# Kernel optimization log

Hardware: AMD Instinct MI355X
Metric: run time of the kernel (lower is better)

Reference implementation:

```python
import jax, jax.numpy as jnp
import numpy as np

EPS = 1e-5

def _leaky(x):
    return jax.nn.leaky_relu(x, 0.2)

def _bn(x, p, axis):
    # p: [4, C] rows = (gamma, beta, running_mean, running_var); inference-mode BN
    g, b, m, v = p
    scale = g * jax.lax.rsqrt(v + EPS)
    shape = [1] * x.ndim
    shape[axis] = -1
    return x * scale.reshape(shape) + (b - m * scale).reshape(shape)

def _graph_feature(x, k):
    # x: [B, C, N] -> edge features [B, 2C, N, k] (knn on -squared-distance, topk largest)
    B, C, N = x.shape
    xx = jnp.sum(x * x, axis=1)                                   # [B, N]
    pd = 2.0 * jnp.einsum('bcn,bcm->bnm', x, x) - xx[:, :, None] - xx[:, None, :]
    idx = jax.lax.top_k(pd, k)[1]                                 # [B, N, k]
    xt = jnp.transpose(x, (0, 2, 1))                              # [B, N, C]
    nb = xt[jnp.arange(B)[:, None, None], idx]                    # [B, N, k, C]
    ctr = xt[:, :, None, :]
    f = jnp.concatenate([nb - ctr, jnp.broadcast_to(ctr, nb.shape)], axis=-1)
    return jnp.transpose(f, (0, 3, 1, 2))                         # [B, 2C, N, k]

def _cbam(x, fc1, fc2, sw):
    # Channel attention (shared MLP on avg+max pooled) then spatial attention (5x5 conv)
    mlp = lambda v: jax.nn.relu(v @ fc1.T) @ fc2.T
    ca = jax.nn.sigmoid(mlp(jnp.mean(x, (2, 3))) + mlp(jnp.max(x, (2, 3))))
    x = x * ca[:, :, None, None]
    s = jnp.concatenate([jnp.mean(x, 1, keepdims=True), jnp.max(x, 1, keepdims=True)], axis=1)
    sa = jax.lax.conv_general_dilated(s, sw, (1, 1), [(2, 2), (2, 2)],
                                      dimension_numbers=('NCHW', 'OIHW', 'NCHW'))
    return x * jax.nn.sigmoid(sa)

def _edge_block(x, k, W, bn, fc1, fc2, sw):
    f = _graph_feature(x, k)                                      # [B, 2C, N, k]
    f = _leaky(_bn(jnp.einsum('oc,bcnk->bonk', W, f), bn, 1))     # 1x1 conv + BN + LeakyReLU
    f = _cbam(f, fc1, fc2, sw)
    return jnp.max(f, axis=-1)                                    # [B, Cout, N]

def _bn_params(key, c):
    k1, k2, k3, k4 = jax.random.split(key, 4)
    g = 1.0 + 0.1 * jax.random.normal(k1, (c,))
    b = 0.1 * jax.random.normal(k2, (c,))
    m = 0.1 * jax.random.normal(k3, (c,))
    v = 0.5 + jax.random.uniform(k4, (c,))
    return jnp.stack([g, b, m, v])

def setup_inputs() -> dict:
    key = jax.random.key(0)
    nrm = lambda i, shape, s: s * jax.random.normal(jax.random.fold_in(key, i), shape, dtype=jnp.float32)
    d = {}
    d['x'] = jax.random.normal(jax.random.fold_in(key, 0), (4, 3, 2048), dtype=jnp.float32)
    d['W1'] = nrm(1, (64, 6), 0.3)
    d['W2'] = nrm(2, (64, 128), 0.15)
    d['W3'] = nrm(3, (128, 128), 0.15)
    d['W4'] = nrm(4, (256, 256), 0.1)
    d['W5'] = nrm(5, (1024, 512), 0.08)
    for i, c in zip(range(1, 6), [64, 64, 128, 256, 1024]):
        d['bn%d' % i] = _bn_params(jax.random.fold_in(key, 10 + i), c)
    d['bn6'] = _bn_params(jax.random.fold_in(key, 16), 512)
    d['bn7'] = _bn_params(jax.random.fold_in(key, 17), 256)
    for j, c in zip(range(1, 5), [64, 64, 128, 256]):
        r = c // 8
        d['ca%d_fc1' % j] = nrm(20 + j, (r, c), 0.2)
        d['ca%d_fc2' % j] = nrm(30 + j, (c, r), 0.2)
        d['sa%d' % j] = nrm(40 + j, (1, 2, 5, 5), 0.2)
    d['lin1_w'] = nrm(50, (512, 2048), 0.05)
    d['lin2_w'] = nrm(51, (256, 512), 0.08)
    d['lin2_b'] = nrm(52, (256,), 0.05)
    d['lin3_w'] = nrm(53, (40, 256), 0.1)
    d['lin3_b'] = nrm(54, (40,), 0.05)
    d['k'] = 20
    return d

def reference(x, W1, bn1, ca1_fc1, ca1_fc2, sa1, W2, bn2, ca2_fc1, ca2_fc2, sa2,
              W3, bn3, ca3_fc1, ca3_fc2, sa3, W4, bn4, ca4_fc1, ca4_fc2, sa4,
              W5, bn5, lin1_w, bn6, lin2_w, lin2_b, bn7, lin3_w, lin3_b, k):
    x1 = _edge_block(x,  k, W1, bn1, ca1_fc1, ca1_fc2, sa1)   # [B, 64, N]
    x2 = _edge_block(x1, k, W2, bn2, ca2_fc1, ca2_fc2, sa2)   # [B, 64, N]
    x3 = _edge_block(x2, k, W3, bn3, ca3_fc1, ca3_fc2, sa3)   # [B, 128, N]
    x4 = _edge_block(x3, k, W4, bn4, ca4_fc1, ca4_fc2, sa4)   # [B, 256, N]
    xc = jnp.concatenate([x1, x2, x3, x4], axis=1)            # [B, 512, N]
    h = _leaky(_bn(jnp.einsum('oc,bcn->bon', W5, xc), bn5, 1))  # [B, 1024, N]
    g = jnp.concatenate([jnp.max(h, axis=-1), jnp.mean(h, axis=-1)], axis=1)  # [B, 2048]
    g = _leaky(_bn(g @ lin1_w.T, bn6, 1))                     # dropout = identity (eval)
    g = _leaky(_bn(g @ lin2_w.T + lin2_b, bn7, 1))
    return g @ lin3_w.T + lin3_b                              # [B, 40]
```

## Files before the change

### kernel.cpp

```cpp
#include <hip/hip_runtime.h>
#include <math.h>

#define BB 4
#define NN 2048
#define KK 20
#define EPSF 1e-5f
#define TR 4

__device__ __forceinline__ float leaky(float x){ return x > 0.f ? x : 0.2f*x; }
__device__ __forceinline__ float sigm(float x){ return 1.f/(1.f+expf(-x)); }

__global__ void k_xx(const float* __restrict__ X, long bstride, int C, float* __restrict__ xx){
  int i = blockIdx.x*blockDim.x + threadIdx.x;
  int b = i >> 11, n = i & (NN-1);
  const float* xb = X + (long)b*bstride;
  float s = 0.f;
  for (int c = 0; c < C; ++c){ float v = xb[c*NN + n]; s += v*v; }
  xx[i] = s;
}

__global__ __launch_bounds__(256) void k_knn(const float* __restrict__ X, long bstride, int C,
                      const float* __restrict__ xx, int* __restrict__ idx){
  __shared__ unsigned int pdrow[TR][NN];
  int rowsPerB = NN/TR;
  int b = blockIdx.x / rowsPerB;
  int r0 = (blockIdx.x % rowsPerB) * TR;
  const float* xb = X + (long)b*bstride;
  int tid = threadIdx.x;

  float acc[4][8];
  #pragma unroll
  for (int r = 0; r < 4; ++r)
    #pragma unroll
    for (int j = 0; j < 8; ++j) acc[r][j] = 0.f;
  for (int c = 0; c < C; ++c){
    const float* xcp = xb + (long)c*NN;
    float4 ctr = *(const float4*)(xcp + r0);
    float v[8];
    #pragma unroll
    for (int j = 0; j < 8; ++j) v[j] = xcp[tid + 256*j];
    #pragma unroll
    for (int j = 0; j < 8; ++j){
      acc[0][j] = fmaf(ctr.x, v[j], acc[0][j]);
      acc[1][j] = fmaf(ctr.y, v[j], acc[1][j]);
      acc[2][j] = fmaf(ctr.z, v[j], acc[2][j]);
      acc[3][j] = fmaf(ctr.w, v[j], acc[3][j]);
    }
  }
  float xxr[4];
  #pragma unroll
  for (int r = 0; r < 4; ++r) xxr[r] = xx[b*NN + r0 + r];
  #pragma unroll
  for (int j = 0; j < 8; ++j){
    int m = tid + 256*j;
    float xxm = xx[b*NN + m];
    #pragma unroll
    for (int r = 0; r < 4; ++r){
      float pd = 2.f*acc[r][j] - xxr[r] - xxm;
      unsigned u = __float_as_uint(pd);
      u ^= (u & 0x80000000u) ? 0xFFFFFFFFu : 0x80000000u;
      pdrow[r][m] = u;
    }
  }
  __syncthreads();

  int wave = tid >> 6, lane = tid & 63;
  int r = wave;
  unsigned long long k1 = 0ull, k2 = 0ull;
  #pragma unroll
  for (int j = 0; j < 32; ++j){
    int m = lane + (j<<6);
    unsigned long long key = ((unsigned long long)pdrow[r][m] << 11) | (unsigned)(2047 - m);
    if (key > k1){ k2 = k1; k1 = key; }
    else if (key > k2){ k2 = key; }
  }
  unsigned removed = 0u;
  int* orow = idx + ((long)b*NN + r0 + r)*KK;
  for (int sel = 0; sel < KK; ++sel){
    unsigned long long g = k1;
    #pragma unroll
    for (int off = 32; off; off >>= 1){
      unsigned long long o = __shfl_xor(g, off);
      if (o > g) g = o;
    }
    int gm = 2047 - (int)(g & 2047u);
    if (lane == 0) orow[sel] = gm;
    if ((gm & 63) == lane){
      removed |= 1u << (gm >> 6);
      k1 = k2; k2 = 0ull;
      if (k1 == 0ull){
        #pragma unroll
        for (int j = 0; j < 32; ++j){
          if (removed & (1u << j)) continue;
          int m = lane + (j<<6);
          unsigned long long key = ((unsigned long long)pdrow[r][m] << 11) | (unsigned)(2047 - m);
          if (key > k1){ k2 = k1; k1 = key; }
          else if (key > k2){ k2 = key; }
        }
      }
    }
  }
}

__global__ void k_proj(const float* __restrict__ X, long bstride, int C, int Cout,
                       const float* __restrict__ W, const float* __restrict__ bn,
                       float* __restrict__ Pg, float* __restrict__ PgT,
                       float* __restrict__ Pc, float* __restrict__ PcT){
  int nb = NN/256;
  int t = blockIdx.x;
  int nchunk = t % nb; t /= nb;
  int o = t % Cout; int b = t / Cout;
  int m = nchunk*256 + threadIdx.x;
  const float* xb = X + (long)b*bstride;
  float a1 = 0.f, a2 = 0.f;
  for (int c = 0; c < C; ++c){
    float v  = xb[c*NN + m];
    float wl = W[o*2*C + c], wr = W[o*2*C + C + c];
    a1 += wl*v; a2 += (wr - wl)*v;
  }
  float gg = bn[o], bb = bn[Cout+o], mn = bn[2*Cout+o], vv = bn[3*Cout+o];
  float scale = gg * rsqrtf(vv + EPSF);
  float bias  = bb - mn*scale;
  float pg = scale*a1;
  float pc = scale*a2 + bias;
  Pg [((long)b*Cout + o)*NN + m] = pg;
  PgT[((long)b*NN + m)*Cout + o] = pg;
  Pc [((long)b*Cout + o)*NN + m] = pc;
  PcT[((long)b*NN + m)*Cout + o] = pc;
}

__global__ void k_cstats(const float* __restrict__ Pg, const float* __restrict__ Pc,
                         const int* __restrict__ idx, int Cout,
                         float* __restrict__ cmean, float* __restrict__ cmax){
  int b = blockIdx.x / Cout, o = blockIdx.x % Cout;
  const float* pg = Pg + ((long)b*Cout + o)*NN;
  const float* pc = Pc + ((long)b*Cout + o)*NN;
  const int* id = idx + (long)b*NN*KK;
  int tid = threadIdx.x;
  float s = 0.f, mx = -INFINITY;
  for (int i = tid; i < NN*KK; i += 256){
    int n = i / KK;
    int iv = id[i];
    float v = leaky(pg[iv] + pc[n]);
    s += v; mx = fmaxf(mx, v);
  }
  __shared__ float ss[256], sm[256];
  ss[tid] = s; sm[tid] = mx; __syncthreads();
  for (int st = 128; st; st >>= 1){
    if (tid < st){ ss[tid] += ss[tid+st]; sm[tid] = fmaxf(sm[tid], sm[tid+st]); }
    __syncthreads();
  }
  if (tid == 0){ cmean[blockIdx.x] = ss[0]/(float)(NN*KK); cmax[blockIdx.x] = sm[0]; }
}

__global__ void k_catt(const float* __restrict__ cmean, const float* __restrict__ cmax,
                       const float* __restrict__ fc1, const float* __restrict__ fc2,
                       int Cout, int r, float* __restrict__ ca){
  int b = blockIdx.x, tid = threadIdx.x;
  __shared__ float h1m[32], h1x[32];
  __shared__ float mv[256], xv[256];
  if (tid < Cout){ mv[tid] = cmean[b*Cout+tid]; xv[tid] = cmax[b*Cout+tid]; }
  __syncthreads();
  if (tid < r){
    float am = 0.f, ax = 0.f;
    for (int c = 0; c < Cout; ++c){ float w = fc1[tid*Cout+c]; am += w*mv[c]; ax += w*xv[c]; }
    h1m[tid] = fmaxf(am, 0.f); h1x[tid] = fmaxf(ax, 0.f);
  }
  __syncthreads();
  if (tid < Cout){
    float a = 0.f;
    for (int j = 0; j < r; ++j) a += fc2[tid*r+j]*(h1m[j] + h1x[j]);
    ca[b*Cout+tid] = sigm(a);
  }
}

__global__ void k_sstats(const float* __restrict__ PgT, const float* __restrict__ PcT,
                         const int* __restrict__ idx, const float* __restrict__ ca,
                         int Cout, float* __restrict__ s){
  long i = (long)blockIdx.x*256 + threadIdx.x;
  int kk = (int)(i % KK); long t = i / KK; int n = (int)(t % NN); int b = (int)(t / NN);
  int iv = idx[((long)b*NN + n)*KK + kk];
  const float4* pg4 = (const float4*)(PgT + ((long)b*NN + iv)*Cout);
  const float4* pc4 = (const float4*)(PcT + ((long)b*NN + n)*Cout);
  const float4* ca4 = (const float4*)(ca + b*Cout);
  float sum = 0.f, mx = -INFINITY;
  int q = Cout >> 2;
  for (int o = 0; o < q; ++o){
    float4 a = pg4[o], c = pc4[o], w = ca4[o];
    float v0 = leaky(a.x + c.x) * w.x;
    float v1 = leaky(a.y + c.y) * w.y;
    float v2 = leaky(a.z + c.z) * w.z;
    float v3 = leaky(a.w + c.w) * w.w;
    sum += v0; mx = fmaxf(mx, v0);
    sum += v1; mx = fmaxf(mx, v1);
    sum += v2; mx = fmaxf(mx, v2);
    sum += v3; mx = fmaxf(mx, v3);
  }
  s[((long)b*2*NN + n)*KK + kk]      = sum/(float)Cout;
  s[((long)b*2*NN + NN + n)*KK + kk] = mx;
}

__global__ void k_sconv(const float* __restrict__ s, const float* __restrict__ sw,
                        float* __restrict__ sa){
  long i = (long)blockIdx.x*256 + threadIdx.x;
  int kk = (int)(i % KK); long t = i / KK; int n = (int)(t % NN); int b = (int)(t / NN);
  float acc = 0.f;
  for (int ci = 0; ci < 2; ++ci)
    for (int dy = 0; dy < 5; ++dy){
      int nn = n + dy - 2; if (nn < 0 || nn >= NN) continue;
      for (int dx = 0; dx < 5; ++dx){
        int kx = kk + dx - 2; if (kx < 0 || kx >= KK) continue;
        acc += sw[ci*25 + dy*5 + dx] * s[((long)b*2*NN + ci*NN + nn)*KK + kx];
      }
    }
  sa[i] = sigm(acc);
}

__global__ void k_final(const float* __restrict__ Pg, const float* __restrict__ Pc,
                        const int* __restrict__ idx, const float* __restrict__ ca,
                        const float* __restrict__ sa, int Cout, int outoff,
                        float* __restrict__ xc){
  long i = (long)blockIdx.x*256 + threadIdx.x;
  int n = (int)(i % NN); long t = i / NN; int o = (int)(t % Cout); int b = (int)(t / Cout);
  const float* pg = Pg + ((long)b*Cout + o)*NN;
  float pcv = Pc[((long)b*Cout + o)*NN + n];
  float cav = ca[b*Cout + o];
  const int* id   = idx + ((long)b*NN + n)*KK;
  const float* sb = sa  + ((long)b*NN + n)*KK;
  float mx = -INFINITY;
  for (int kk = 0; kk < KK; ++kk){
    float v = leaky(pg[id[kk]] + pcv) * cav * sb[kk];
    mx = fmaxf(mx, v);
  }
  xc[((long)b*512 + outoff + o)*NN + n] = mx;
}

__global__ __launch_bounds__(256) void k_gemm5(const float* __restrict__ xc, const float* __restrict__ W5,
                        const float* __restrict__ bn5, float* __restrict__ gpart){
  __shared__ float xs[32][128];
  __shared__ float wsd[64][33];
  int t = blockIdx.x;
  int nb = t & 15; t >>= 4;
  int ob = t & 15; int b = t >> 4;
  int n0 = nb << 7, o0 = ob << 6;
  int tid = threadIdx.x;
  int tx = tid & 15, ty = tid >> 4;
  const float* xb = xc + (long)b*512*NN + n0;

  float acc[4][8];
  #pragma unroll
  for (int i = 0; i < 4; ++i)
    #pragma unroll
    for (int j = 0; j < 8; ++j) acc[i][j] = 0.f;

  for (int cc = 0; cc < 16; ++cc){
    {
      int col4 = tid & 31;
      int ci0 = tid >> 5;
      #pragma unroll
      for (int q = 0; q < 4; ++q){
        int ci = ci0 + (q << 3);
        float4 v = *(const float4*)(xb + (long)(cc*32 + ci)*NN + (col4 << 2));
        *(float4*)&xs[ci][col4 << 2] = v;
      }
    }
    {
      int ci4 = tid & 7;
      int oi0 = tid >> 3;
      #pragma unroll
      for (int q = 0; q < 2; ++q){
        int oi = oi0 + (q << 5);
        float4 w = *(const float4*)(W5 + (long)(o0 + oi)*512 + cc*32 + (ci4 << 2));
        wsd[oi][(ci4 << 2) + 0] = w.x;
        wsd[oi][(ci4 << 2) + 1] = w.y;
        wsd[oi][(ci4 << 2) + 2] = w.z;
        wsd[oi][(ci4 << 2) + 3] = w.w;
      }
    }
    __syncthreads();
    #pragma unroll 8
    for (int ci = 0; ci < 32; ++ci){
      float4 xa = *(const float4*)&xs[ci][tx << 2];
      float4 xc2 = *(const float4*)&xs[ci][64 + (tx << 2)];
      float w0 = wsd[(ty << 2) + 0][ci];
      float w1 = wsd[(ty << 2) + 1][ci];
      float w2 = wsd[(ty << 2) + 2][ci];
      float w3 = wsd[(ty << 2) + 3][ci];
      acc[0][0] = fmaf(w0, xa.x, acc[0][0]); acc[0][1] = fmaf(w0, xa.y, acc[0][1]);
      acc[0][2] = fmaf(w0, xa.z, acc[0][2]); acc[0][3] = fmaf(w0, xa.w, acc[0][3]);
      acc[0][4] = fmaf(w0, xc2.x, acc[0][4]); acc[0][5] = fmaf(w0, xc2.y, acc[0][5]);
      acc[0][6] = fmaf(w0, xc2.z, acc[0][6]); acc[0][7] = fmaf(w0, xc2.w, acc[0][7]);
      acc[1][0] = fmaf(w1, xa.x, acc[1][0]); acc[1][1] = fmaf(w1, xa.y, acc[1][1]);
      acc[1][2] = fmaf(w1, xa.z, acc[1][2]); acc[1][3] = fmaf(w1, xa.w, acc[1][3]);
      acc[1][4] = fmaf(w1, xc2.x, acc[1][4]); acc[1][5] = fmaf(w1, xc2.y, acc[1][5]);
      acc[1][6] = fmaf(w1, xc2.z, acc[1][6]); acc[1][7] = fmaf(w1, xc2.w, acc[1][7]);
      acc[2][0] = fmaf(w2, xa.x, acc[2][0]); acc[2][1] = fmaf(w2, xa.y, acc[2][1]);
      acc[2][2] = fmaf(w2, xa.z, acc[2][2]); acc[2][3] = fmaf(w2, xa.w, acc[2][3]);
      acc[2][4] = fmaf(w2, xc2.x, acc[2][4]); acc[2][5] = fmaf(w2, xc2.y, acc[2][5]);
      acc[2][6] = fmaf(w2, xc2.z, acc[2][6]); acc[2][7] = fmaf(w2, xc2.w, acc[2][7]);
      acc[3][0] = fmaf(w3, xa.x, acc[3][0]); acc[3][1] = fmaf(w3, xa.y, acc[3][1]);
      acc[3][2] = fmaf(w3, xa.z, acc[3][2]); acc[3][3] = fmaf(w3, xa.w, acc[3][3]);
      acc[3][4] = fmaf(w3, xc2.x, acc[3][4]); acc[3][5] = fmaf(w3, xc2.y, acc[3][5]);
      acc[3][6] = fmaf(w3, xc2.z, acc[3][6]); acc[3][7] = fmaf(w3, xc2.w, acc[3][7]);
    }
    __syncthreads();
  }

  float psum[4], pmax[4];
  #pragma unroll
  for (int oo = 0; oo < 4; ++oo){
    int o = o0 + (ty << 2) + oo;
    float scale = bn5[o] * rsqrtf(bn5[3072 + o] + EPSF);
    float bias  = bn5[1024 + o] - bn5[2048 + o] * scale;
    float s = 0.f, mx = -INFINITY;
    #pragma unroll
    for (int j = 0; j < 8; ++j){
      float v = leaky(fmaf(scale, acc[oo][j], bias));
      s += v; mx = fmaxf(mx, v);
    }
    psum[oo] = s; pmax[oo] = mx;
  }
  __syncthreads();
  float* ps = &xs[0][0];
  float* pm = ps + 64*17;
  #pragma unroll
  for (int oo = 0; oo < 4; ++oo){
    int o = (ty << 2) + oo;
    ps[o*17 + tx] = psum[oo];
    pm[o*17 + tx] = pmax[oo];
  }
  __syncthreads();
  if (tid < 64){
    float s = 0.f, mx = -INFINITY;
    #pragma unroll
    for (int j = 0; j < 16; ++j){
      s += ps[tid*17 + j];
      mx = fmaxf(mx, pm[tid*17 + j]);
    }
    long base = ((long)(b*16 + nb))*1024 + o0 + tid;
    gpart[base] = s;
    gpart[65536 + base] = mx;
  }
}

__global__ void k_pool2(const float* __restrict__ gpart, float* __restrict__ g){
  int i = blockIdx.x*256 + threadIdx.x;
  int b = i >> 10, o = i & 1023;
  float s = 0.f, mx = -INFINITY;
  for (int nb = 0; nb < 16; ++nb){
    s += gpart[((long)(b*16 + nb))*1024 + o];
    mx = fmaxf(mx, gpart[65536 + ((long)(b*16 + nb))*1024 + o]);
  }
  g[b*2048 + o] = mx;
  g[b*2048 + 1024 + o] = s * (1.f/2048.f);
}

__global__ void k_dense(const float* __restrict__ in, const float* __restrict__ w,
                        const float* __restrict__ bias, const float* __restrict__ bnp,
                        int Cin, int Cout, float* __restrict__ out){
  int b = blockIdx.x / Cout, j = blockIdx.x % Cout;
  int tid = threadIdx.x;
  float a = 0.f;
  for (int c = tid; c < Cin; c += 256) a += w[(long)j*Cin + c]*in[(long)b*Cin + c];
  __shared__ float ss[256];
  ss[tid] = a; __syncthreads();
  for (int st = 128; st; st >>= 1){
    if (tid < st) ss[tid] += ss[tid+st];
    __syncthreads();
  }
  if (tid == 0){
    float v = ss[0];
    if (bias) v += bias[j];
    if (bnp){
      float scale = bnp[j]*rsqrtf(bnp[3*Cout+j] + EPSF);
      float bb    = bnp[Cout+j] - bnp[2*Cout+j]*scale;
      v = leaky(v*scale + bb);
    }
    out[b*Cout + j] = v;
  }
}

extern "C" void kernel_launch(void* const* d_in, const int* in_sizes, int n_in,
                              void* d_out, int out_size, void* d_ws, size_t ws_size,
                              hipStream_t stream){
  (void)in_sizes; (void)n_in; (void)out_size;
  const float* x  = (const float*)d_in[0];
  const float* Wb[4]  = {(const float*)d_in[1], (const float*)d_in[2], (const float*)d_in[3], (const float*)d_in[4]};
  const float* W5     = (const float*)d_in[5];
  const float* bnb[4] = {(const float*)d_in[6], (const float*)d_in[7], (const float*)d_in[8], (const float*)d_in[9]};
  const float* bn5    = (const float*)d_in[10];
  const float* bn6    = (const float*)d_in[11];
  const float* bn7    = (const float*)d_in[12];
  const float* fc1b[4] = {(const float*)d_in[13], (const float*)d_in[16], (const float*)d_in[19], (const float*)d_in[22]};
  const float* fc2b[4] = {(const float*)d_in[14], (const float*)d_in[17], (const float*)d_in[20], (const float*)d_in[23]};
  const float* swb[4]  = {(const float*)d_in[15], (const float*)d_in[18], (const float*)d_in[21], (const float*)d_in[24]};
  const float* lin1_w = (const float*)d_in[25];
  const float* lin2_w = (const float*)d_in[26];
  const float* lin2_b = (const float*)d_in[27];
  const float* lin3_w = (const float*)d_in[28];
  const float* lin3_b = (const float*)d_in[29];

  float* ws = (float*)d_ws;
  float* xc = ws;
  float* tb = ws + (size_t)BB*512*NN;
  float* xx   = tb;
  int*   idx  = (int*)(tb + 8192);
  float* Pg   = tb + 8192 + 163840;
  float* PgT  = Pg  + 2097152;
  float* Pc   = PgT + 2097152;
  float* PcT  = Pc  + 2097152;
  float* cmean = PcT + 2097152;
  float* cmax  = cmean + 1024;
  float* ca    = cmax + 1024;
  float* s     = ca + 1024;
  float* sa    = s + 327680;
  float* gpart = tb;
  float* g  = tb + 131072;
  float* t1 = g + 8192;
  float* t2 = t1 + 2048;
  size_t needed = ((size_t)BB*512*NN + 9055232) * 4;
  if (ws_size < needed) return;

  const int Cin [4] = {3, 64, 64, 128};
  const int Cout[4] = {64, 64, 128, 256};
  const int inoff[4]  = {0, 0, 64, 128};
  const int outoff[4] = {0, 64, 128, 256};

  for (int blk = 0; blk < 4; ++blk){
    const float* Xp; long bstr;
    if (blk == 0){ Xp = x; bstr = 3l*NN; }
    else { Xp = xc + (long)inoff[blk]*NN; bstr = 512l*NN; }
    int C = Cin[blk], Co = Cout[blk];
    hipLaunchKernelGGL(k_xx,    dim3(BB*NN/256), dim3(256), 0, stream, Xp, bstr, C, xx);
    hipLaunchKernelGGL(k_knn,   dim3(BB*NN/TR),  dim3(256), 0, stream, Xp, bstr, C, xx, idx);
    hipLaunchKernelGGL(k_proj,  dim3(BB*Co*(NN/256)), dim3(256), 0, stream, Xp, bstr, C, Co, Wb[blk], bnb[blk], Pg, PgT, Pc, PcT);
    hipLaunchKernelGGL(k_cstats, dim3(BB*Co), dim3(256), 0, stream, Pg, Pc, idx, Co, cmean, cmax);
    hipLaunchKernelGGL(k_catt,  dim3(BB), dim3(256), 0, stream, cmean, cmax, fc1b[blk], fc2b[blk], Co, Co/8, ca);
    hipLaunchKernelGGL(k_sstats, dim3(BB*NN*KK/256), dim3(256), 0, stream, PgT, PcT, idx, ca, Co, s);
    hipLaunchKernelGGL(k_sconv, dim3(BB*NN*KK/256), dim3(256), 0, stream, s, swb[blk], sa);
    hipLaunchKernelGGL(k_final, dim3(BB*Co*NN/256), dim3(256), 0, stream, Pg, Pc, idx, ca, sa, Co, outoff[blk], xc);
  }
  hipLaunchKernelGGL(k_gemm5, dim3(BB*16*16), dim3(256), 0, stream, xc, W5, bn5, gpart);
  hipLaunchKernelGGL(k_pool2, dim3(16), dim3(256), 0, stream, gpart, g);
  hipLaunchKernelGGL(k_dense, dim3(BB*512), dim3(256), 0, stream, g,  lin1_w, (const float*)nullptr, bn6, 2048, 512, t1);
  hipLaunchKernelGGL(k_dense, dim3(BB*256), dim3(256), 0, stream, t1, lin2_w, lin2_b, bn7, 512, 256, t2);
  hipLaunchKernelGGL(k_dense, dim3(BB*40),  dim3(256), 0, stream, t2, lin3_w, lin3_b, (const float*)nullptr, 256, 40, (float*)d_out);
}
```

Baseline: 1.223 ms.

## Add shared-memory tiled projection kernel for edge blocks 2-4

Adds a tiled GEMM-style projection kernel that stages 32-channel slices of the input and the weights in shared memory. Each thread computes a 4x8 register tile for both the neighbor and center projections, and all four outputs, including the transposed copies, are written as float4. It replaces the per-thread naive dot-product kernel, which re-read weights and inputs from global memory with uncoalesced transposed stores, for blocks whose channel count is a multiple of 32/64. Block 0 with C=3 keeps the old kernel.

```diff
diff --git a/kernel.cpp b/kernel.cpp
--- a/kernel.cpp
+++ b/kernel.cpp
@@ -127,6 +127,113 @@
   PgT[((long)b*NN + m)*Cout + o] = pg;
   Pc [((long)b*Cout + o)*NN + m] = pc;
   PcT[((long)b*NN + m)*Cout + o] = pc;
+}
+
+__global__ __launch_bounds__(256) void k_proj_t(const float* __restrict__ X, long bstride, int C, int Cout,
+                         const float* __restrict__ W, const float* __restrict__ bn,
+                         float* __restrict__ Pg, float* __restrict__ PgT,
+                         float* __restrict__ Pc, float* __restrict__ PcT){
+  __shared__ float xs[32][128];
+  __shared__ float wls[64][33];
+  __shared__ float wds[64][33];
+  int t = blockIdx.x;
+  int nb = t & 15; t >>= 4;
+  int nob = Cout >> 6;
+  int ob = t % nob; int b = t / nob;
+  int n0 = nb << 7, o0 = ob << 6;
+  int tid = threadIdx.x;
+  int tx = tid & 15, ty = tid >> 4;
+  const float* xb = X + (long)b*bstride + n0;
+
+  float ag[4][8], ac[4][8];
+  #pragma unroll
+  for (int i = 0; i < 4; ++i)
+    #pragma unroll
+    for (int j = 0; j < 8; ++j){ ag[i][j] = 0.f; ac[i][j] = 0.f; }
+
+  for (int cc = 0; cc < C; cc += 32){
+    {
+      int col4 = tid & 31;
+      int ci0 = tid >> 5;
+      #pragma unroll
+      for (int q = 0; q < 4; ++q){
+        int ci = ci0 + (q << 3);
+        float4 v = *(const float4*)(xb + (long)(cc + ci)*NN + (col4 << 2));
+        *(float4*)&xs[ci][col4 << 2] = v;
+      }
+    }
+    {
+      int ci4 = tid & 7;
+      int oi0 = tid >> 3;
+      #pragma unroll
+      for (int q = 0; q < 2; ++q){
+        int oi = oi0 + (q << 5);
+        const float* wrow = W + (long)(o0 + oi)*2*C + cc + (ci4 << 2);
+        float4 wl = *(const float4*)(wrow);
+        float4 wr = *(const float4*)(wrow + C);
+        wls[oi][(ci4 << 2) + 0] = wl.x;
+        wls[oi][(ci4 << 2) + 1] = wl.y;
+        wls[oi][(ci4 << 2) + 2] = wl.z;
+        wls[oi][(ci4 << 2) + 3] = wl.w;
+        wds[oi][(ci4 << 2) + 0] = wr.x - wl.x;
+        wds[oi][(ci4 << 2) + 1] = wr.y - wl.y;
+        wds[oi][(ci4 << 2) + 2] = wr.z - wl.z;
+        wds[oi][(ci4 << 2) + 3] = wr.w - wl.w;
+      }
+    }
+    __syncthreads();
+    #pragma unroll 8
+    for (int ci = 0; ci < 32; ++ci){
+      float4 xa  = *(const float4*)&xs[ci][tx << 2];
+      float4 xc2 = *(const float4*)&xs[ci][64 + (tx << 2)];
+      #pragma unroll
+      for (int oo = 0; oo < 4; ++oo){
+        float wl = wls[(ty << 2) + oo][ci];
+        float wd = wds[(ty << 2) + oo][ci];
+        ag[oo][0] = fmaf(wl, xa.x, ag[oo][0]); ag[oo][1] = fmaf(wl, xa.y, ag[oo][1]);
+        ag[oo][2] = fmaf(wl, xa.z, ag[oo][2]); ag[oo][3] = fmaf(wl, xa.w, ag[oo][3]);
+        ag[oo][4] = fmaf(wl, xc2.x, ag[oo][4]); ag[oo][5] = fmaf(wl, xc2.y, ag[oo][5]);
+        ag[oo][6] = fmaf(wl, xc2.z, ag[oo][6]); ag[oo][7] = fmaf(wl, xc2.w, ag[oo][7]);
+        ac[oo][0] = fmaf(wd, xa.x, ac[oo][0]); ac[oo][1] = fmaf(wd, xa.y, ac[oo][1]);
+        ac[oo][2] = fmaf(wd, xa.z, ac[oo][2]); ac[oo][3] = fmaf(wd, xa.w, ac[oo][3]);
+        ac[oo][4] = fmaf(wd, xc2.x, ac[oo][4]); ac[oo][5] = fmaf(wd, xc2.y, ac[oo][5]);
+        ac[oo][6] = fmaf(wd, xc2.z, ac[oo][6]); ac[oo][7] = fmaf(wd, xc2.w, ac[oo][7]);
+      }
+    }
+    __syncthreads();
+  }
+
+  float scl[4], bia[4];
+  #pragma unroll
+  for (int oo = 0; oo < 4; ++oo){
+    int o = o0 + (ty << 2) + oo;
+    scl[oo] = bn[o] * rsqrtf(bn[3*Cout + o] + EPSF);
+    bia[oo] = bn[Cout + o] - bn[2*Cout + o]*scl[oo];
+  }
+  #pragma unroll
+  for (int oo = 0; oo < 4; ++oo){
+    long rb = ((long)b*Cout + o0 + (ty << 2) + oo)*NN + n0;
+    float4 g0 = {scl[oo]*ag[oo][0], scl[oo]*ag[oo][1], scl[oo]*ag[oo][2], scl[oo]*ag[oo][3]};
+    float4 g1 = {scl[oo]*ag[oo][4], scl[oo]*ag[oo][5], scl[oo]*ag[oo][6], scl[oo]*ag[oo][7]};
+    float4 c0 = {fmaf(scl[oo], ac[oo][0], bia[oo]), fmaf(scl[oo], ac[oo][1], bia[oo]),
+                 fmaf(scl[oo], ac[oo][2], bia[oo]), fmaf(scl[oo], ac[oo][3], bia[oo])};
+    float4 c1 = {fmaf(scl[oo], ac[oo][4], bia[oo]), fmaf(scl[oo], ac[oo][5], bia[oo]),
+                 fmaf(scl[oo], ac[oo][6], bia[oo]), fmaf(scl[oo], ac[oo][7], bia[oo])};
+    *(float4*)(Pg + rb + (tx << 2))      = g0;
+    *(float4*)(Pg + rb + 64 + (tx << 2)) = g1;
+    *(float4*)(Pc + rb + (tx << 2))      = c0;
+    *(float4*)(Pc + rb + 64 + (tx << 2)) = c1;
+  }
+  #pragma unroll
+  for (int j = 0; j < 8; ++j){
+    int n = n0 + ((j < 4) ? (tx << 2) + j : 64 + (tx << 2) + (j - 4));
+    long rb = ((long)b*NN + n)*Cout + o0 + (ty << 2);
+    float4 tg = {scl[0]*ag[0][j], scl[1]*ag[1][j], scl[2]*ag[2][j], scl[3]*ag[3][j]};
+    float4 tc = {fmaf(scl[0], ac[0][j], bia[0]), fmaf(scl[1], ac[1][j], bia[1]),
+                 fmaf(scl[2], ac[2][j], bia[2]), fmaf(scl[3], ac[3][j], bia[3])};
+    *(float4*)(PgT + rb) = tg;
+    *(float4*)(PcT + rb) = tc;
+  }
 }
 
 __global__ void k_cstats(const float* __restrict__ Pg, const float* __restrict__ Pc,
@@ -433,7 +540,11 @@
     int C = Cin[blk], Co = Cout[blk];
     hipLaunchKernelGGL(k_xx,    dim3(BB*NN/256), dim3(256), 0, stream, Xp, bstr, C, xx);
     hipLaunchKernelGGL(k_knn,   dim3(BB*NN/TR),  dim3(256), 0, stream, Xp, bstr, C, xx, idx);
-    hipLaunchKernelGGL(k_proj,  dim3(BB*Co*(NN/256)), dim3(256), 0, stream, Xp, bstr, C, Co, Wb[blk], bnb[blk], Pg, PgT, Pc, PcT);
+    if (blk == 0){
+      hipLaunchKernelGGL(k_proj,  dim3(BB*Co*(NN/256)), dim3(256), 0, stream, Xp, bstr, C, Co, Wb[blk], bnb[blk], Pg, PgT, Pc, PcT);
+    } else {
+      hipLaunchKernelGGL(k_proj_t, dim3(BB*(Co>>6)*16), dim3(256), 0, stream, Xp, bstr, C, Co, Wb[blk], bnb[blk], Pg, PgT, Pc, PcT);
+    }
     hipLaunchKernelGGL(k_cstats, dim3(BB*Co), dim3(256), 0, stream, Pg, Pc, idx, Co, cmean, cmax);
     hipLaunchKernelGGL(k_catt,  dim3(BB), dim3(256), 0, stream, cmean, cmax, fc1b[blk], fc2b[blk], Co, Co/8, ca);
     hipLaunchKernelGGL(k_sstats, dim3(BB*NN*KK/256), dim3(256), 0, stream, PgT, PcT, idx, ca, Co, s);
```

Result: faster. 1.110 ms (-9.2%).
